# Performance work log

Measured on AMD Instinct MI355X. Metric: run time of the kernel, lower is better.

## Reference

```python
import jax, jax.numpy as jnp
import numpy as np

B, D, T = 32, 256, 2048
L, K = 8, 1024


def setup_inputs() -> dict:
    key = jax.random.key(0)
    k1, k2 = jax.random.split(key)
    x = jax.random.normal(k1, (B, D, T), dtype=jnp.float32)
    codebooks = jax.random.normal(k2, (L, K, D), dtype=jnp.float32)
    return {"x": x, "codebooks": codebooks}


def reference(x, codebooks):
    """Residual VQ: per layer, cdist + argmin + gather, subtract, accumulate.

    x: (B, D, T) latents; codebooks: (L, K, D).
    Returns (output (B, D, T), indices (B, L, T)).
    """
    b, d, t = x.shape
    r0 = jnp.transpose(x, (0, 2, 1)).reshape(-1, d)  # (N, D), N = B*T

    def step(residual, W):
        # squared euclidean distance: |r|^2 - 2 r.W^T + |W|^2  -> (N, K)
        dist2 = (jnp.sum(residual * residual, axis=-1, keepdims=True)
                 - 2.0 * residual @ W.T
                 + jnp.sum(W * W, axis=-1))
        idx = jnp.argmin(dist2, axis=-1)          # (N,)
        q = W[idx]                                 # gather (N, D)
        return residual - q, (q, idx)

    _, (qs, idxs) = jax.lax.scan(step, r0, codebooks)
    out = jnp.sum(qs, axis=0).reshape(b, t, d)     # sum over layers
    out = jnp.transpose(out, (0, 2, 1))            # (B, D, T)
    indices = jnp.transpose(idxs.reshape(codebooks.shape[0], b, t), (1, 0, 2))  # (B, L, T)
    return out, indices
```

## Files before the change

kernel.cpp:

```cpp
#include <hip/hip_runtime.h>
#include <cmath>

constexpr int Bb = 32, Dd = 256, Tt = 2048, Ll = 8, Kk = 1024;
constexpr int VT = 64;
constexpr int KT = 64;
constexpr int ROWU = 264;
constexpr int HALF_USH = KT * ROWU;
constexpr int TILE_BYTES = 2 * HALF_USH * 2;
constexpr int CHUNKS = TILE_BYTES / 16 / 64;

typedef __attribute__((ext_vector_type(8))) short short8;
typedef __attribute__((ext_vector_type(4))) float f32x4;

__device__ __forceinline__ ushort f2bf(float x) {
    union { float f; uint32_t u; } v{x};
    uint32_t r = v.u + 0x7fffu + ((v.u >> 16) & 1u);
    return (ushort)(r >> 16);
}
__device__ __forceinline__ float bf2f(ushort h) {
    union { uint32_t u; float f; } v{((uint32_t)h) << 16};
    return v.f;
}
__device__ __forceinline__ void gl_lds16(const void* g, void* l) {
    __builtin_amdgcn_global_load_lds(
        (const __attribute__((address_space(1))) unsigned int*)g,
        (__attribute__((address_space(3))) unsigned int*)l, 16, 0, 0);
}

__global__ void prep_kernel(const float* __restrict__ cb, float* __restrict__ wn,
                            ushort* __restrict__ sp) {
    const int code = blockIdx.x;
    const int lane = threadIdx.x;
    const int l = code >> 10, kk = code & 1023, kt = kk >> 6, kr = kk & 63;
    const float4 v = ((const float4*)(cb + (size_t)code * Dd))[lane];
    float s = v.x * v.x + v.y * v.y + v.z * v.z + v.w * v.w;
#pragma unroll
    for (int off = 32; off > 0; off >>= 1) s += __shfl_down(s, off, 64);
    if (lane == 0) wn[code] = s;

    float f[4] = {v.x, v.y, v.z, v.w};
    ushort hs[4], ls[4];
#pragma unroll
    for (int i = 0; i < 4; ++i) {
        hs[i] = f2bf(f[i]);
        ls[i] = f2bf(f[i] - bf2f(hs[i]));
    }
    ushort* base = sp + (size_t)(l * 16 + kt) * (2 * HALF_USH) + kr * ROWU + lane * 4;
    *(ushort4*)base               = make_ushort4(hs[0], hs[1], hs[2], hs[3]);
    *(ushort4*)(base + HALF_USH)  = make_ushort4(ls[0], ls[1], ls[2], ls[3]);
}

__launch_bounds__(256, 2)
__global__ void rvq_kernel(const float* __restrict__ x, const float* __restrict__ cb,
                           const float* __restrict__ wn, const ushort* __restrict__ sp,
                           float* __restrict__ out, float* __restrict__ oidx) {
    __shared__ __align__(16) ushort Btile[2 * HALF_USH];
    __shared__ int   sidx[VT];
    __shared__ int   cnt[VT];
    __shared__ int   cand[VT * 32];

    const int tid = threadIdx.x;
    const int w = tid >> 6, lane = tid & 63;
    const int c = lane & 15;
    const int q = lane >> 4;
    const int b = blockIdx.x >> 5, t0 = (blockIdx.x & 31) * VT;
    const int myrow = 16 * w + c;
    const int t_a = t0 + myrow;

    float R_[8][8];
    {
        const float* xb = x + (size_t)b * Dd * Tt + t_a;
#pragma unroll
        for (int s = 0; s < 8; ++s)
#pragma unroll
            for (int j = 0; j < 8; ++j)
                R_[s][j] = xb[(size_t)(32 * s + 8 * q + j) * Tt];
    }

    for (int l = 0; l < Ll; ++l) {
        const float*  cbl = cb + (size_t)l * Kk * Dd;
        const float*  wnl = wn + l * Kk;
        const ushort* spl = sp + (size_t)l * 16 * (2 * HALF_USH);

        short8 ah[8], al[8];
#pragma unroll
        for (int s = 0; s < 8; ++s)
#pragma unroll
            for (int j = 0; j < 8; ++j) {
                float v = R_[s][j];
                ushort h = f2bf(v);
                ah[s][j] = (short)h;
                al[s][j] = (short)f2bf(v - bf2f(h));
            }

        float d1[4], d2[4]; int i1[4], i2[4];
#pragma unroll
        for (int i = 0; i < 4; ++i) { d1[i] = __builtin_inff(); d2[i] = __builtin_inff(); i1[i] = 0; i2[i] = 0; }

        for (int kt = 0; kt < 16; ++kt) {
            __syncthreads();
            {
                const char* gsrc = (const char*)spl + (size_t)kt * TILE_BYTES;
                char* ldst = (char*)Btile;
                for (int ch = w; ch < CHUNKS; ch += 4)
                    gl_lds16(gsrc + ch * 1024 + lane * 16, ldst + ch * 1024);
            }
            __syncthreads();

            float wnv[4];
#pragma unroll
            for (int sub = 0; sub < 4; ++sub) wnv[sub] = wnl[kt * 64 + sub * 16 + c];

            f32x4 hh[4], hl[4], lh[4];
#pragma unroll
            for (int sub = 0; sub < 4; ++sub) { hh[sub] = (f32x4)0.f; hl[sub] = (f32x4)0.f; lh[sub] = (f32x4)0.f; }

#pragma unroll
            for (int s = 0; s < 8; ++s) {
                const ushort* bp = Btile + s * 32 + q * 8;
                short8 bf[4];
#pragma unroll
                for (int sub = 0; sub < 4; ++sub)
                    bf[sub] = *(const short8*)(bp + (sub * 16 + c) * ROWU);
#pragma unroll
                for (int sub = 0; sub < 4; ++sub)
                    hh[sub] = __builtin_amdgcn_mfma_f32_16x16x32_bf16(ah[s], bf[sub], hh[sub], 0, 0, 0);
#pragma unroll
                for (int sub = 0; sub < 4; ++sub)
                    lh[sub] = __builtin_amdgcn_mfma_f32_16x16x32_bf16(al[s], bf[sub], lh[sub], 0, 0, 0);
#pragma unroll
                for (int sub = 0; sub < 4; ++sub)
                    bf[sub] = *(const short8*)(bp + HALF_USH + (sub * 16 + c) * ROWU);
#pragma unroll
                for (int sub = 0; sub < 4; ++sub)
                    hl[sub] = __builtin_amdgcn_mfma_f32_16x16x32_bf16(ah[s], bf[sub], hl[sub], 0, 0, 0);
            }
#pragma unroll
            for (int sub = 0; sub < 4; ++sub) {
                const int kbase = kt * 64 + sub * 16 + c;
#pragma unroll
                for (int i = 0; i < 4; ++i) {
                    float acc = hh[sub][i] + hl[sub][i] + lh[sub][i];
                    float d = fmaf(-2.f, acc, wnv[sub]);
                    bool lt1 = d < d1[i], lt2 = d < d2[i];
                    d2[i] = lt1 ? d1[i] : (lt2 ? d : d2[i]);
                    i2[i] = lt1 ? i1[i] : (lt2 ? kbase : i2[i]);
                    d1[i] = lt1 ? d : d1[i];
                    i1[i] = lt1 ? kbase : i1[i];
                }
            }
        }

        __syncthreads();
        float* Rcp = (float*)Btile;
        {
            float* dst = Rcp + myrow * ROWU + 8 * q;
#pragma unroll
            for (int s = 0; s < 8; ++s) {
                float4 lo4 = {R_[s][0], R_[s][1], R_[s][2], R_[s][3]};
                float4 hi4 = {R_[s][4], R_[s][5], R_[s][6], R_[s][7]};
                *(float4*)(dst + 32 * s)     = lo4;
                *(float4*)(dst + 32 * s + 4) = hi4;
            }
        }
        if (tid < VT) cnt[tid] = 0;

        float bmin[4];
#pragma unroll
        for (int i = 0; i < 4; ++i) {
            float md = d1[i];
#pragma unroll
            for (int off = 1; off < 16; off <<= 1) {
                float od = __shfl_xor(md, off, 64);
                md = od < md ? od : md;
            }
            bmin[i] = md;
        }
        __syncthreads();

#pragma unroll
        for (int i = 0; i < 4; ++i) {
            const int row = 16 * w + 4 * q + i;
            const float thr = bmin[i] + 0.20f;
            if (d1[i] <= thr) { int s_ = atomicAdd(&cnt[row], 1); cand[row * 32 + s_] = i1[i]; }
            if (d2[i] <= thr) { int s_ = atomicAdd(&cnt[row], 1); cand[row * 32 + s_] = i2[i]; }
        }
        __syncthreads();

        if (tid < VT) {
            const int row = tid;
            const int n = cnt[row];
            int bi = cand[row * 32];
            if (n > 1) {
                const float* rp = Rcp + row * ROWU;
                float rn = 0.f;
                for (int i = 0; i < Dd / 4; ++i) {
                    float4 r4 = *(const float4*)(rp + 4 * i);
                    rn += r4.x * r4.x + r4.y * r4.y + r4.z * r4.z + r4.w * r4.w;
                }
                float bd = __builtin_inff(); bi = 0x7fffffff;
                for (int j = 0; j < n; ++j) {
                    const int cc = cand[row * 32 + j];
                    const float* wp = cbl + (size_t)cc * Dd;
                    float dot = 0.f;
                    for (int d = 0; d < Dd; ++d)
                        dot = fmaf(rp[d], wp[d], dot);
                    const float dist = (rn - 2.0f * dot) + wnl[cc];
                    if (dist < bd || (dist == bd && cc < bi)) { bd = dist; bi = cc; }
                }
            }
            sidx[row] = bi;
            oidx[((size_t)b * Ll + l) * Tt + t0 + row] = (float)bi;
        }
        __syncthreads();

        {
            const int cc = sidx[myrow];
            const float* wp = cbl + (size_t)cc * Dd + 8 * q;
#pragma unroll
            for (int s = 0; s < 8; ++s) {
                float4 w0 = *(const float4*)(wp + 32 * s);
                float4 w1 = *(const float4*)(wp + 32 * s + 4);
                R_[s][0] -= w0.x; R_[s][1] -= w0.y; R_[s][2] -= w0.z; R_[s][3] -= w0.w;
                R_[s][4] -= w1.x; R_[s][5] -= w1.y; R_[s][6] -= w1.z; R_[s][7] -= w1.w;
            }
        }
    }

    {
        const float* xb = x + (size_t)b * Dd * Tt + t_a;
        float* ob = out + (size_t)b * Dd * Tt + t_a;
#pragma unroll
        for (int s = 0; s < 8; ++s)
#pragma unroll
            for (int j = 0; j < 8; ++j) {
                size_t off = (size_t)(32 * s + 8 * q + j) * Tt;
                ob[off] = xb[off] - R_[s][j];
            }
    }
}

extern "C" void kernel_launch(void* const* d_in, const int* in_sizes, int n_in,
                              void* d_out, int out_size, void* d_ws, size_t ws_size,
                              hipStream_t stream) {
    const float* x  = (const float*)d_in[0];
    const float* cb = (const float*)d_in[1];
    float* out  = (float*)d_out;
    float* oidx = out + (size_t)Bb * Dd * Tt;
    float*  wnbuf = (float*)d_ws;
    ushort* spbuf = (ushort*)((char*)d_ws + 32768);

    prep_kernel<<<Ll * Kk, 64, 0, stream>>>(cb, wnbuf, spbuf);
    rvq_kernel<<<(Bb * Tt) / VT, 256, 0, stream>>>(x, cb, wnbuf, spbuf, out, oidx);
}
```

Before: 1.158 ms.

## Switch to 32x32x16 MFMA with packed-key top-2 and bf16-split residual registers

Replaces the 16x16x32 MFMA tiling with 32x32x16 MFMAs, so each wave covers 32 rows by 32 codes. The residual is kept only as bf16 hi/lo register pairs instead of fp32 plus per-layer conversion. Top-2 tracking packs an order-preserving distance with the tile index into a single uint key, which cuts compare and select work. The exact rescoring rebuilds the fp32 residual from x and the stored index history, and the output is recomputed from the history. This trades register pressure and some recompute in rare rescoring paths for fewer MFMA issues and cheaper argmin bookkeeping, though the residual loses precision through the bf16 hi/lo representation.

```diff
diff --git a/kernel.cpp b/kernel.cpp
--- a/kernel.cpp
+++ b/kernel.cpp
@@ -3,14 +3,13 @@
 
 constexpr int Bb = 32, Dd = 256, Tt = 2048, Ll = 8, Kk = 1024;
 constexpr int VT = 64;
-constexpr int KT = 64;
 constexpr int ROWU = 264;
-constexpr int HALF_USH = KT * ROWU;
+constexpr int HALF_USH = 64 * ROWU;
 constexpr int TILE_BYTES = 2 * HALF_USH * 2;
 constexpr int CHUNKS = TILE_BYTES / 16 / 64;
 
 typedef __attribute__((ext_vector_type(8))) short short8;
-typedef __attribute__((ext_vector_type(4))) float f32x4;
+typedef __attribute__((ext_vector_type(16))) float f32x16;
 
 __device__ __forceinline__ ushort f2bf(float x) {
     union { float f; uint32_t u; } v{x};
@@ -20,6 +19,14 @@
 __device__ __forceinline__ float bf2f(ushort h) {
     union { uint32_t u; float f; } v{((uint32_t)h) << 16};
     return v.f;
+}
+__device__ __forceinline__ uint fmap(float f) {
+    uint b = __float_as_uint(f);
+    return b ^ (0x80000000u | (uint)((int)b >> 31));
+}
+__device__ __forceinline__ float funmap(uint u) {
+    uint b = (u & 0x80000000u) ? (u ^ 0x80000000u) : ~u;
+    return __uint_as_float(b);
 }
 __device__ __forceinline__ void gl_lds16(const void* g, void* l) {
     __builtin_amdgcn_global_load_lds(
@@ -55,26 +62,32 @@
                            const float* __restrict__ wn, const ushort* __restrict__ sp,
                            float* __restrict__ out, float* __restrict__ oidx) {
     __shared__ __align__(16) ushort Btile[2 * HALF_USH];
-    __shared__ int   sidx[VT];
-    __shared__ int   cnt[VT];
-    __shared__ int   cand[VT * 32];
+    __shared__ int    cnt[VT];
+    __shared__ ushort cand[VT * 64];
+    __shared__ ushort hist[Ll][VT];
 
     const int tid = threadIdx.x;
     const int w = tid >> 6, lane = tid & 63;
-    const int c = lane & 15;
-    const int q = lane >> 4;
+    const int n = lane & 31;
+    const int h = lane >> 5;
+    const int rh = w >> 1;
+    const int ch = w & 1;
     const int b = blockIdx.x >> 5, t0 = (blockIdx.x & 31) * VT;
-    const int myrow = 16 * w + c;
-    const int t_a = t0 + myrow;
-
-    float R_[8][8];
+    const int row32 = 32 * rh + n;
+    const int t_a = t0 + row32;
+
+    short8 ahf[16], alf[16];
     {
         const float* xb = x + (size_t)b * Dd * Tt + t_a;
 #pragma unroll
-        for (int s = 0; s < 8; ++s)
-#pragma unroll
-            for (int j = 0; j < 8; ++j)
-                R_[s][j] = xb[(size_t)(32 * s + 8 * q + j) * Tt];
+        for (int t = 0; t < 16; ++t)
+#pragma unroll
+            for (int j = 0; j < 8; ++j) {
+                float v = xb[(size_t)(16 * t + 8 * h + j) * Tt];
+                ushort hi = f2bf(v);
+                ahf[t][j] = (short)hi;
+                alf[t][j] = (short)f2bf(v - bf2f(hi));
+            }
     }
 
     for (int l = 0; l < Ll; ++l) {
@@ -82,147 +95,116 @@
         const float*  wnl = wn + l * Kk;
         const ushort* spl = sp + (size_t)l * 16 * (2 * HALF_USH);
 
-        short8 ah[8], al[8];
-#pragma unroll
-        for (int s = 0; s < 8; ++s)
-#pragma unroll
-            for (int j = 0; j < 8; ++j) {
-                float v = R_[s][j];
-                ushort h = f2bf(v);
-                ah[s][j] = (short)h;
-                al[s][j] = (short)f2bf(v - bf2f(h));
-            }
-
-        float d1[4], d2[4]; int i1[4], i2[4];
-#pragma unroll
-        for (int i = 0; i < 4; ++i) { d1[i] = __builtin_inff(); d2[i] = __builtin_inff(); i1[i] = 0; i2[i] = 0; }
+        uint u1[16], u2[16];
+#pragma unroll
+        for (int e = 0; e < 16; ++e) { u1[e] = 0xFFFFFFFFu; u2[e] = 0xFFFFFFFFu; }
 
         for (int kt = 0; kt < 16; ++kt) {
             __syncthreads();
             {
                 const char* gsrc = (const char*)spl + (size_t)kt * TILE_BYTES;
                 char* ldst = (char*)Btile;
-                for (int ch = w; ch < CHUNKS; ch += 4)
-                    gl_lds16(gsrc + ch * 1024 + lane * 16, ldst + ch * 1024);
+                for (int c2 = w; c2 < CHUNKS; c2 += 4)
+                    gl_lds16(gsrc + c2 * 1024 + lane * 16, ldst + c2 * 1024);
             }
             __syncthreads();
 
-            float wnv[4];
-#pragma unroll
-            for (int sub = 0; sub < 4; ++sub) wnv[sub] = wnl[kt * 64 + sub * 16 + c];
-
-            f32x4 hh[4], hl[4], lh[4];
-#pragma unroll
-            for (int sub = 0; sub < 4; ++sub) { hh[sub] = (f32x4)0.f; hl[sub] = (f32x4)0.f; lh[sub] = (f32x4)0.f; }
-
-#pragma unroll
-            for (int s = 0; s < 8; ++s) {
-                const ushort* bp = Btile + s * 32 + q * 8;
-                short8 bf[4];
-#pragma unroll
-                for (int sub = 0; sub < 4; ++sub)
-                    bf[sub] = *(const short8*)(bp + (sub * 16 + c) * ROWU);
-#pragma unroll
-                for (int sub = 0; sub < 4; ++sub)
-                    hh[sub] = __builtin_amdgcn_mfma_f32_16x16x32_bf16(ah[s], bf[sub], hh[sub], 0, 0, 0);
-#pragma unroll
-                for (int sub = 0; sub < 4; ++sub)
-                    lh[sub] = __builtin_amdgcn_mfma_f32_16x16x32_bf16(al[s], bf[sub], lh[sub], 0, 0, 0);
-#pragma unroll
-                for (int sub = 0; sub < 4; ++sub)
-                    bf[sub] = *(const short8*)(bp + HALF_USH + (sub * 16 + c) * ROWU);
-#pragma unroll
-                for (int sub = 0; sub < 4; ++sub)
-                    hl[sub] = __builtin_amdgcn_mfma_f32_16x16x32_bf16(ah[s], bf[sub], hl[sub], 0, 0, 0);
-            }
-#pragma unroll
-            for (int sub = 0; sub < 4; ++sub) {
-                const int kbase = kt * 64 + sub * 16 + c;
-#pragma unroll
-                for (int i = 0; i < 4; ++i) {
-                    float acc = hh[sub][i] + hl[sub][i] + lh[sub][i];
-                    float d = fmaf(-2.f, acc, wnv[sub]);
-                    bool lt1 = d < d1[i], lt2 = d < d2[i];
-                    d2[i] = lt1 ? d1[i] : (lt2 ? d : d2[i]);
-                    i2[i] = lt1 ? i1[i] : (lt2 ? kbase : i2[i]);
-                    d1[i] = lt1 ? d : d1[i];
-                    i1[i] = lt1 ? kbase : i1[i];
-                }
-            }
-        }
-
-        __syncthreads();
-        float* Rcp = (float*)Btile;
-        {
-            float* dst = Rcp + myrow * ROWU + 8 * q;
-#pragma unroll
-            for (int s = 0; s < 8; ++s) {
-                float4 lo4 = {R_[s][0], R_[s][1], R_[s][2], R_[s][3]};
-                float4 hi4 = {R_[s][4], R_[s][5], R_[s][6], R_[s][7]};
-                *(float4*)(dst + 32 * s)     = lo4;
-                *(float4*)(dst + 32 * s + 4) = hi4;
-            }
-        }
+            const float wnv = wnl[kt * 64 + ch * 32 + n];
+
+            f32x16 hh = (f32x16)0.f, hl = (f32x16)0.f, lh = (f32x16)0.f;
+#pragma unroll
+            for (int t = 0; t < 16; ++t) {
+                const ushort* bp = Btile + (ch * 32 + n) * ROWU + 16 * t + 8 * h;
+                short8 bh = *(const short8*)bp;
+                short8 bl = *(const short8*)(bp + HALF_USH);
+                hh = __builtin_amdgcn_mfma_f32_32x32x16_bf16(ahf[t], bh, hh, 0, 0, 0);
+                lh = __builtin_amdgcn_mfma_f32_32x32x16_bf16(alf[t], bh, lh, 0, 0, 0);
+                hl = __builtin_amdgcn_mfma_f32_32x32x16_bf16(ahf[t], bl, hl, 0, 0, 0);
+            }
+#pragma unroll
+            for (int e = 0; e < 16; ++e) {
+                float dist = fmaf(-2.f, hh[e] + hl[e] + lh[e], wnv);
+                uint key = (fmap(dist) & 0xFFFFFFF0u) | (uint)kt;
+                uint mx = u1[e] > key ? u1[e] : key;
+                u2[e] = u2[e] < mx ? u2[e] : mx;
+                u1[e] = u1[e] < key ? u1[e] : key;
+            }
+        }
+
+        __syncthreads();
         if (tid < VT) cnt[tid] = 0;
-
-        float bmin[4];
-#pragma unroll
-        for (int i = 0; i < 4; ++i) {
-            float md = d1[i];
-#pragma unroll
-            for (int off = 1; off < 16; off <<= 1) {
-                float od = __shfl_xor(md, off, 64);
-                md = od < md ? od : md;
-            }
-            bmin[i] = md;
-        }
-        __syncthreads();
-
-#pragma unroll
-        for (int i = 0; i < 4; ++i) {
-            const int row = 16 * w + 4 * q + i;
-            const float thr = bmin[i] + 0.20f;
-            if (d1[i] <= thr) { int s_ = atomicAdd(&cnt[row], 1); cand[row * 32 + s_] = i1[i]; }
-            if (d2[i] <= thr) { int s_ = atomicAdd(&cnt[row], 1); cand[row * 32 + s_] = i2[i]; }
+        __syncthreads();
+
+#pragma unroll
+        for (int e = 0; e < 16; ++e) {
+            const int rloc = (e & 3) + 8 * (e >> 2) + 4 * h;
+            const int row = 32 * rh + rloc;
+            uint bm = u1[e];
+#pragma unroll
+            for (int off = 1; off < 32; off <<= 1) {
+                uint o = (uint)__shfl_xor((int)bm, off, 64);
+                bm = o < bm ? o : bm;
+            }
+            const uint thr = fmap(funmap(bm) + 0.15f) | 0xFu;
+            if (u1[e] <= thr) {
+                int s_ = atomicAdd(&cnt[row], 1);
+                if (s_ < 64) cand[row * 64 + s_] = (ushort)((u1[e] & 15u) * 64 + ch * 32 + n);
+            }
+            if (u2[e] <= thr) {
+                int s_ = atomicAdd(&cnt[row], 1);
+                if (s_ < 64) cand[row * 64 + s_] = (ushort)((u2[e] & 15u) * 64 + ch * 32 + n);
+            }
         }
         __syncthreads();
 
         if (tid < VT) {
             const int row = tid;
-            const int n = cnt[row];
-            int bi = cand[row * 32];
-            if (n > 1) {
-                const float* rp = Rcp + row * ROWU;
+            const int nc = cnt[row] < 64 ? cnt[row] : 64;
+            int bi = cand[row * 64];
+            if (nc > 1) {
+                float* Rrow = (float*)Btile + row * ROWU;
+                const float* xrow = x + (size_t)b * Dd * Tt + t0 + row;
+                for (int d = 0; d < Dd; ++d) Rrow[d] = xrow[(size_t)d * Tt];
+                for (int j = 0; j < l; ++j) {
+                    const float* qp = cb + ((size_t)j * Kk + hist[j][row]) * Dd;
+                    for (int d = 0; d < Dd; ++d) Rrow[d] -= qp[d];
+                }
                 float rn = 0.f;
                 for (int i = 0; i < Dd / 4; ++i) {
-                    float4 r4 = *(const float4*)(rp + 4 * i);
+                    float4 r4 = *(const float4*)(Rrow + 4 * i);
                     rn += r4.x * r4.x + r4.y * r4.y + r4.z * r4.z + r4.w * r4.w;
                 }
                 float bd = __builtin_inff(); bi = 0x7fffffff;
-                for (int j = 0; j < n; ++j) {
-                    const int cc = cand[row * 32 + j];
+                for (int c2 = 0; c2 < nc; ++c2) {
+                    const int cc = cand[row * 64 + c2];
                     const float* wp = cbl + (size_t)cc * Dd;
                     float dot = 0.f;
                     for (int d = 0; d < Dd; ++d)
-                        dot = fmaf(rp[d], wp[d], dot);
+                        dot = fmaf(Rrow[d], wp[d], dot);
                     const float dist = (rn - 2.0f * dot) + wnl[cc];
                     if (dist < bd || (dist == bd && cc < bi)) { bd = dist; bi = cc; }
                 }
             }
-            sidx[row] = bi;
+            hist[l][row] = (ushort)bi;
             oidx[((size_t)b * Ll + l) * Tt + t0 + row] = (float)bi;
         }
         __syncthreads();
 
         {
-            const int cc = sidx[myrow];
-            const float* wp = cbl + (size_t)cc * Dd + 8 * q;
-#pragma unroll
-            for (int s = 0; s < 8; ++s) {
-                float4 w0 = *(const float4*)(wp + 32 * s);
-                float4 w1 = *(const float4*)(wp + 32 * s + 4);
-                R_[s][0] -= w0.x; R_[s][1] -= w0.y; R_[s][2] -= w0.z; R_[s][3] -= w0.w;
-                R_[s][4] -= w1.x; R_[s][5] -= w1.y; R_[s][6] -= w1.z; R_[s][7] -= w1.w;
+            const int cc = hist[l][row32];
+            const float* wp = cbl + (size_t)cc * Dd;
+#pragma unroll
+            for (int t = 0; t < 16; ++t) {
+                float4 q0 = *(const float4*)(wp + 16 * t + 8 * h);
+                float4 q1 = *(const float4*)(wp + 16 * t + 8 * h + 4);
+                float qv[8] = {q0.x, q0.y, q0.z, q0.w, q1.x, q1.y, q1.z, q1.w};
+#pragma unroll
+                for (int j = 0; j < 8; ++j) {
+                    float v = (bf2f((ushort)ahf[t][j]) + bf2f((ushort)alf[t][j])) - qv[j];
+                    ushort hi = f2bf(v);
+                    ahf[t][j] = (short)hi;
+                    alf[t][j] = (short)f2bf(v - bf2f(hi));
+                }
             }
         }
     }
@@ -231,12 +213,25 @@
         const float* xb = x + (size_t)b * Dd * Tt + t_a;
         float* ob = out + (size_t)b * Dd * Tt + t_a;
 #pragma unroll
-        for (int s = 0; s < 8; ++s)
+        for (int t = 0; t < 16; ++t) {
+            float xv[8], v[8];
 #pragma unroll
             for (int j = 0; j < 8; ++j) {
-                size_t off = (size_t)(32 * s + 8 * q + j) * Tt;
-                ob[off] = xb[off] - R_[s][j];
-            }
+                xv[j] = xb[(size_t)(16 * t + 8 * h + j) * Tt];
+                v[j] = xv[j];
+            }
+            for (int lay = 0; lay < Ll; ++lay) {
+                const float* qp = cb + ((size_t)lay * Kk + hist[lay][row32]) * Dd
+                                  + 16 * t + 8 * h;
+                float4 q0 = *(const float4*)qp;
+                float4 q1 = *(const float4*)(qp + 4);
+                v[0] -= q0.x; v[1] -= q0.y; v[2] -= q0.z; v[3] -= q0.w;
+                v[4] -= q1.x; v[5] -= q1.y; v[6] -= q1.z; v[7] -= q1.w;
+            }
+#pragma unroll
+            for (int j = 0; j < 8; ++j)
+                ob[(size_t)(16 * t + 8 * h + j) * Tt] = xv[j] - v[j];
+        }
     }
 }
 
```

Result: slower. 2.968 ms (+156.2%).
